# Kernel optimization log

Measured on AMD Instinct MI355X. Metric: run time of the kernel, lower is better.

Reference implementation:

```python
import jax, jax.numpy as jnp
import numpy as np


def _propagate(x, src, dst, norm, n):
    # PyG propagate with aggr='add': out[dst_e] += norm_e * x[src_e]
    return jax.ops.segment_sum(x[src] * norm[:, None], dst, num_segments=n)


def _dconv(x, w, b, row, col, norm_out, norm_in, n):
    # DConv with K=2: w has shape (2, 2, c_in, c_out)
    # k=0 term: identity for both diffusion directions
    h = x @ w[0, 0] + x @ w[1, 0]
    # k=1 term: 1-hop diffusion, forward edges and flipped edges
    tx_o = _propagate(x, row, col, norm_out, n)  # out-degree normalized walk
    tx_i = _propagate(x, col, row, norm_in, n)   # edge_index.flip([0]) walk
    h = h + tx_o @ w[0, 1] + tx_i @ w[1, 1]
    return h + b


def reference(x, edge_index, edge_weight, w_lin2, b_lin2, w_z, b_z, w_r, b_r, w_h, b_h, w_out, b_out):
    n = x.shape[0]
    row, col = edge_index[0], edge_index[1]
    # degrees from weighted adjacency (same as to_dense_adj row/col sums)
    deg_out = jax.ops.segment_sum(edge_weight, row, num_segments=n)
    deg_in = jax.ops.segment_sum(edge_weight, col, num_segments=n)
    norm_out = (1.0 / deg_out)[row]
    norm_in = (1.0 / deg_in)[row]

    h = x.reshape(n, -1)                      # Flatten: (n, 24)
    h = jax.nn.sigmoid(h @ w_lin2 + b_lin2)   # (n, hidden)

    # DCRNN GRU cell, hidden state initialized to zeros (single step)
    h0 = jnp.zeros_like(h)
    xh = jnp.concatenate([h, h0], axis=1)     # (n, 2*hidden)
    z = jax.nn.sigmoid(_dconv(xh, w_z, b_z, row, col, norm_out, norm_in, n))
    r = jax.nn.sigmoid(_dconv(xh, w_r, b_r, row, col, norm_out, norm_in, n))
    xhr = jnp.concatenate([h, h0 * r], axis=1)
    h_tilde = jnp.tanh(_dconv(xhr, w_h, b_h, row, col, norm_out, norm_in, n))
    h_new = z * h0 + (1.0 - z) * h_tilde

    return jax.nn.sigmoid(h_new) @ w_out + b_out  # (n, out_periods)


def setup_inputs() -> dict:
    key = jax.random.key(0)
    ks = jax.random.split(key, 12)
    N, DEG, HID, OUTP, WIN, HOR = 100000, 8, 64, 12, 2, 12
    E = N * DEG

    x = jax.random.normal(ks[0], (N, WIN, HOR), dtype=jnp.float32)

    # random edges + a ring so every node has out-degree>=1 and in-degree>=1
    e_rand = N * (DEG - 1)
    row_r = jax.random.randint(ks[1], (e_rand,), 0, N, dtype=jnp.int32)
    col_r = jax.random.randint(ks[2], (e_rand,), 0, N, dtype=jnp.int32)
    ring = jnp.arange(N, dtype=jnp.int32)
    row = jnp.concatenate([row_r, ring])
    col = jnp.concatenate([col_r, (ring + 1) % N])
    edge_index = jnp.stack([row, col])  # (2, E)
    edge_weight = jax.random.uniform(ks[3], (E,), minval=0.5, maxval=1.5, dtype=jnp.float32)

    def lin_w(k, fi, fo):
        return jax.random.normal(k, (fi, fo), jnp.float32) / np.float32(np.sqrt(fi))

    def dconv_w(k, cin, cout):
        return jax.random.normal(k, (2, 2, cin, cout), jnp.float32) / np.float32(np.sqrt(cin))

    cin = 2 * HID
    return {
        "x": x,
        "edge_index": edge_index,
        "edge_weight": edge_weight,
        "w_lin2": lin_w(ks[4], WIN * HOR, HID),
        "b_lin2": jnp.zeros((HID,), jnp.float32),
        "w_z": dconv_w(ks[5], cin, HID),
        "b_z": jnp.zeros((HID,), jnp.float32),
        "w_r": dconv_w(ks[6], cin, HID),
        "b_r": jnp.zeros((HID,), jnp.float32),
        "w_h": dconv_w(ks[7], cin, HID),
        "b_h": jnp.zeros((HID,), jnp.float32),
        "w_out": lin_w(ks[8], HID, OUTP),
        "b_out": jnp.zeros((OUTP,), jnp.float32),
    }
```

## Files before the change

kernel.cpp:

```cpp
#include <hip/hip_runtime.h>


typedef unsigned long long ull;
typedef unsigned short ushort;
typedef unsigned int uint;
typedef __attribute__((ext_vector_type(8))) short bf16x8;
typedef __attribute__((ext_vector_type(4))) float f32x4;

#define BSZ    64
#define CAP    768
#define CHUNK  4096
#define MAXBKT 2048

__device__ __forceinline__ float sigmoid_f(float x) {
    return 1.0f / (1.0f + __expf(-x));
}
__device__ __forceinline__ float tanh_f(float x) {
    float ax = fabsf(x);
    float e = __expf(-2.0f * ax);
    float t = (1.0f - e) / (1.0f + e);
    return copysignf(t, x);
}
__device__ __forceinline__ ushort f2bf(float f) {
    unsigned u = __float_as_uint(f);
    return (ushort)((u + 0x7FFF + ((u >> 16) & 1)) >> 16);
}
__device__ __forceinline__ float bf2f(ushort s) {
    return __uint_as_float(((unsigned)s) << 16);
}

__global__ void init_kernel(uint* __restrict__ gcur, int nbkt) {
    int t = blockIdx.x * 1024 + threadIdx.x;
    if (t < 2 * nbkt) gcur[t] = (uint)(t % nbkt) * CAP;
}

__global__ void __launch_bounds__(256) mega1_kernel(
        const int* __restrict__ row, const int* __restrict__ col,
        const float* __restrict__ ew, int E,
        uint* __restrict__ gcur, ull* __restrict__ pkbuf,
        int nbkt, int nslot,
        const float* __restrict__ x, const float* __restrict__ Wl,
        const float* __restrict__ bl, ushort* __restrict__ hb, int N,
        const float* __restrict__ wz, const float* __restrict__ bz,
        const float* __restrict__ wh, const float* __restrict__ bh,
        ushort* __restrict__ Wp, float* __restrict__ bc, int SB, int LB) {
    __shared__ float Ws[24 * 64];
    __shared__ float bs[64];
    __shared__ uint hist[MAXBKT];
    __shared__ uint base_s[MAXBKT];
    int bx = blockIdx.x;
    const int t = threadIdx.x;

    if (bx < SB) {
        const int d  = bx & 1;
        const int e0 = (bx >> 1) * CHUNK;
        const int* key = d ? row : col;
        const int* oth = d ? col : row;
        for (int i = t; i < nbkt; i += 256) hist[i] = 0;
        __syncthreads();
#pragma unroll
        for (int j = 0; j < CHUNK / 256; ++j) {
            int e = e0 + j * 256 + t;
            if (e < E) atomicAdd(&hist[key[e] >> 6], 1u);
        }
        __syncthreads();
        for (int i = t; i < nbkt; i += 256) {
            uint c = hist[i];
            base_s[i] = c ? atomicAdd(&gcur[d * nbkt + i], c) : 0u;
            hist[i] = 0;
        }
        __syncthreads();
#pragma unroll
        for (int j = 0; j < CHUNK / 256; ++j) {
            int e = e0 + j * 256 + t;
            if (e < E) {
                int k   = key[e];
                int bkt = k >> 6;
                uint w15 = (uint)(ew[e] * 16384.0f + 0.5f);
                uint s = base_s[bkt] + atomicAdd(&hist[bkt], 1u);
                if (s < ((uint)bkt + 1u) * CAP)
                    pkbuf[(size_t)d * nslot + s] =
                        ((ull)(uint)oth[e] << 32) |
                        ((uint)(k & (BSZ - 1)) << 15) | w15;
            }
        }
        return;
    }
    bx -= SB;
    if (bx < LB) {
        for (int i = t; i < 384; i += 256)
            ((float4*)Ws)[i] = ((const float4*)Wl)[i];
        if (t < 64) bs[t] = bl[t];
        __syncthreads();
        int gid = bx * 256 + t;
        int n = gid >> 6;
        int c = gid & 63;
        if (n >= N) return;
        const float* xr = x + (size_t)n * 24;
        float acc = bs[c];
#pragma unroll
        for (int k4 = 0; k4 < 6; ++k4) {
            float4 xv = *(const float4*)(xr + k4 * 4);
            acc = fmaf(xv.x, Ws[(k4 * 4 + 0) * 64 + c], acc);
            acc = fmaf(xv.y, Ws[(k4 * 4 + 1) * 64 + c], acc);
            acc = fmaf(xv.z, Ws[(k4 * 4 + 2) * 64 + c], acc);
            acc = fmaf(xv.w, Ws[(k4 * 4 + 3) * 64 + c], acc);
        }
        hb[(size_t)n * 64 + c] = f2bf(sigmoid_f(acc));
        return;
    }
    bx -= LB;
    int i = bx * 256 + t;
    if (bx == 0 && t < 128) bc[t] = (t < 64) ? bz[t] : bh[t - 64];
    if (i >= 6 * 8 * 64 * 8) return;
    int j    = i & 7;
    int lane = (i >> 3) & 63;
    int ct   = (i >> 9) & 7;
    int kt   = i >> 12;
    int k = kt * 32 + 8 * (lane >> 4) + j;
    int c = ct * 16 + (lane & 15);
    const float* w = (c < 64) ? wz : wh;
    int cc = c & 63;
    float v;
    if (k < 64)        v = w[(0 * 128 + k) * 64 + cc] + w[(2 * 128 + k) * 64 + cc];
    else if (k < 128)  v = w[(1 * 128 + (k - 64)) * 64 + cc];
    else               v = w[(3 * 128 + (k - 128)) * 64 + cc];
    Wp[i] = f2bf(v);
}

__global__ void __launch_bounds__(256) sort_kernel(
        const uint* __restrict__ gcur, const ull* __restrict__ pkbuf,
        uint* __restrict__ srt, int* __restrict__ beg, int* __restrict__ end,
        float* __restrict__ rdi, float* __restrict__ rdo,
        int nbkt, int nslot, int N) {
    __shared__ uint hist[BSZ];
    __shared__ uint cur[BSZ];
    __shared__ float sdeg[BSZ];
    const int b = blockIdx.x, d = blockIdx.y, t = threadIdx.x;
    if (t < BSZ) { hist[t] = 0; sdeg[t] = 0.0f; }
    __syncthreads();
    uint cnt = gcur[d * nbkt + b] - (uint)b * CAP;
    if (cnt > CAP) cnt = CAP;
    const ull* rec = pkbuf + (size_t)d * nslot + (size_t)b * CAP;
    for (uint i = t; i < cnt; i += 256) {
        ull r = rec[i];
        uint dl = (uint)(r >> 15) & (BSZ - 1);
        atomicAdd(&hist[dl], 1u);
        atomicAdd(&sdeg[dl], (float)(uint)(r & 0x7FFFu));
    }
    __syncthreads();
    if (t < BSZ) {
        int v = (int)hist[t];
        int x = v;
#pragma unroll
        for (int off = 1; off < BSZ; off <<= 1) {
            int y = __shfl_up(x, off, 64);
            if (t >= off) x += y;
        }
        uint p = (uint)(x - v);
        cur[t] = p;
        int n = b * BSZ + t;
        if (n < N) {
            beg[(size_t)d * N + n] = (int)((uint)b * CAP + p);
            end[(size_t)d * N + n] = (int)((uint)b * CAP + p + (uint)v);
            float s = sdeg[t];
            float rv = (s > 0.0f) ? (16384.0f / s) : 0.0f;
            if (d == 0) rdi[n] = rv;
            else        rdo[n] = rv;
        }
    }
    __syncthreads();
    uint* so = srt + (size_t)d * nslot + (size_t)b * CAP;
    for (uint i = t; i < cnt; i += 256) {
        ull r = rec[i];
        uint dl = (uint)(r >> 15) & (BSZ - 1);
        uint p = atomicAdd(&cur[dl], 1u);
        so[p] = (uint)(r >> 32);
    }
}

__global__ void __launch_bounds__(256) gather_kernel(
        const ushort* __restrict__ hb, const uint* __restrict__ srt,
        const int* __restrict__ beg, const int* __restrict__ end,
        const float* __restrict__ rdo, const float* __restrict__ rdi,
        ushort* __restrict__ pob, ushort* __restrict__ pib,
        int nslot, int N) {
    int n = blockIdx.x * 4 + (threadIdx.x >> 6);
    if (n >= N) return;
    const int lane = threadIdx.x & 63;
    const int g    = lane >> 4;
    const int cq   = (lane & 15) * 4;
    const int d    = blockIdx.y;
    const uint* s_ = srt + (size_t)d * nslot;
    int s0 = beg[(size_t)d * N + n];
    int s1 = end[(size_t)d * N + n];

    float a0 = 0.f, a1 = 0.f, a2 = 0.f, a3 = 0.f;
    for (int s = s0; s < s1; s += 8) {
        int sa = s + g, sb = s + 4 + g;
        int ia = (int)s_[(sa < s1) ? sa : s1 - 1];
        int ib = (int)s_[(sb < s1) ? sb : s1 - 1];
        float wa, wb;
        if (d == 0) {
            wa = (sa < s1) ? rdo[ia] : 0.0f;
            wb = (sb < s1) ? rdo[ib] : 0.0f;
        } else {
            wa = (sa < s1) ? 1.0f : 0.0f;
            wb = (sb < s1) ? 1.0f : 0.0f;
        }
        uint2 ha = *(const uint2*)(hb + (size_t)ia * 64 + cq);
        uint2 hc = *(const uint2*)(hb + (size_t)ib * 64 + cq);
        a0 = fmaf(__uint_as_float(ha.x << 16),         wa, a0);
        a1 = fmaf(__uint_as_float(ha.x & 0xFFFF0000u), wa, a1);
        a2 = fmaf(__uint_as_float(ha.y << 16),         wa, a2);
        a3 = fmaf(__uint_as_float(ha.y & 0xFFFF0000u), wa, a3);
        a0 = fmaf(__uint_as_float(hc.x << 16),         wb, a0);
        a1 = fmaf(__uint_as_float(hc.x & 0xFFFF0000u), wb, a1);
        a2 = fmaf(__uint_as_float(hc.y << 16),         wb, a2);
        a3 = fmaf(__uint_as_float(hc.y & 0xFFFF0000u), wb, a3);
    }
    a0 += __shfl_xor(a0, 16, 64); a0 += __shfl_xor(a0, 32, 64);
    a1 += __shfl_xor(a1, 16, 64); a1 += __shfl_xor(a1, 32, 64);
    a2 += __shfl_xor(a2, 16, 64); a2 += __shfl_xor(a2, 32, 64);
    a3 += __shfl_xor(a3, 16, 64); a3 += __shfl_xor(a3, 32, 64);

    if (lane < 16) {
        float m = (d == 0) ? 1.0f : rdi[n];
        uint lo = (uint)f2bf(a0 * m) | ((uint)f2bf(a1 * m) << 16);
        uint hi = (uint)f2bf(a2 * m) | ((uint)f2bf(a3 * m) << 16);
        ushort* dst = (d == 0 ? pob : pib) + (size_t)n * 64 + cq;
        *(uint2*)dst = make_uint2(lo, hi);
    }
}

__global__ void __launch_bounds__(256) gates_kernel(
        const ushort* __restrict__ hb, const ushort* __restrict__ pob,
        const ushort* __restrict__ pib, const ushort* __restrict__ Wp,
        const float* __restrict__ bc, const float* __restrict__ wout,
        const float* __restrict__ bout, float* __restrict__ out, int N) {
    __shared__ float sS[64 * 68];
    __shared__ float sWO[64 * 12];
    const int t    = threadIdx.x;
    const int w    = t >> 6;
    const int lane = t & 63;
    const int n0   = blockIdx.x * 64;

    for (int i = t; i < 64 * 12; i += 256) sWO[i] = wout[i];

    f32x4 acc[8];
#pragma unroll
    for (int ct = 0; ct < 8; ++ct) {
        float bcv = bc[ct * 16 + (lane & 15)];
        acc[ct] = (f32x4){bcv, bcv, bcv, bcv};
    }

    int arow = n0 + w * 16 + (lane & 15);
    if (arow >= N) arow = N - 1;
    const int g8 = (lane >> 4) * 8;
    const ushort* const srcs[3] = {hb, pob, pib};

#pragma unroll
    for (int kc = 0; kc < 6; ++kc) {
        const ushort* src = srcs[kc >> 1];
        bf16x8 a = *(const bf16x8*)(src + (size_t)arow * 64 + (kc & 1) * 32 + g8);
#pragma unroll
        for (int ct = 0; ct < 8; ++ct) {
            bf16x8 b = *(const bf16x8*)(Wp + (size_t)((kc * 8 + ct) * 64 + lane) * 8);
            acc[ct] = __builtin_amdgcn_mfma_f32_16x16x32_bf16(a, b, acc[ct], 0, 0, 0);
        }
    }

    const int rowbase = w * 16 + (lane >> 4) * 4;
    const int colbase = lane & 15;
#pragma unroll
    for (int ct = 0; ct < 4; ++ct) {
#pragma unroll
        for (int r = 0; r < 4; ++r) {
            float zv = sigmoid_f(acc[ct][r]);
            float ht = tanh_f(acc[ct + 4][r]);
            sS[(rowbase + r) * 68 + ct * 16 + colbase] =
                sigmoid_f((1.0f - zv) * ht);
        }
    }
    __syncthreads();

#pragma unroll
    for (int rr = 0; rr < 3; ++rr) {
        int o = rr * 256 + t;
        int node = o / 12;
        int j = o % 12;
        int n = n0 + node;
        if (n >= N) continue;
        float a = bout[j];
#pragma unroll 8
        for (int c2 = 0; c2 < 64; ++c2) a = fmaf(sS[node * 68 + c2], sWO[c2 * 12 + j], a);
        out[(size_t)n * 12 + j] = a;
    }
}

extern "C" void kernel_launch(void* const* d_in, const int* in_sizes, int n_in,
                              void* d_out, int out_size, void* d_ws, size_t ws_size,
                              hipStream_t stream) {
    const float* x      = (const float*)d_in[0];
    const int*   ei     = (const int*)  d_in[1];
    const float* ew     = (const float*)d_in[2];
    const float* w_lin2 = (const float*)d_in[3];
    const float* b_lin2 = (const float*)d_in[4];
    const float* w_z    = (const float*)d_in[5];
    const float* b_z    = (const float*)d_in[6];
    const float* w_h    = (const float*)d_in[9];
    const float* b_h    = (const float*)d_in[10];
    const float* w_out  = (const float*)d_in[11];
    const float* b_out  = (const float*)d_in[12];

    int N = in_sizes[0] / 24;
    int E = in_sizes[1] / 2;
    const int* row = ei;
    const int* col = ei + E;
    int nbkt  = (N + BSZ - 1) / BSZ;
    int nslot = nbkt * CAP;

    ull*    pkbuf = (ull*)d_ws;
    uint*   srt   = (uint*)(pkbuf + 2 * (size_t)nslot);
    ushort* hb    = (ushort*)(srt + 2 * (size_t)nslot);
    ushort* pob   = hb  + (size_t)N * 64;
    ushort* pib   = pob + (size_t)N * 64;
    ushort* Wp    = pib + (size_t)N * 64;
    float*  bc    = (float*)(Wp + 24576);
    float*  rdo   = bc + 128;
    float*  rdi   = rdo + N;
    int*    beg   = (int*)(rdi + N);
    int*    end   = beg + 2 * (size_t)N;
    uint*   gcur  = (uint*)(end + 2 * (size_t)N);

    int SB = 2 * ((E + CHUNK - 1) / CHUNK);
    int LB = (N * 64 + 255) / 256;
    int PB = (6 * 8 * 64 * 8 + 255) / 256;

    init_kernel<<<(2 * nbkt + 1023) / 1024, 1024, 0, stream>>>(gcur, nbkt);
    mega1_kernel<<<SB + LB + PB, 256, 0, stream>>>(
        row, col, ew, E, gcur, pkbuf, nbkt, nslot,
        x, w_lin2, b_lin2, hb, N,
        w_z, b_z, w_h, b_h, Wp, bc, SB, LB);
    sort_kernel<<<dim3(nbkt, 2), 256, 0, stream>>>(gcur, pkbuf, srt, beg, end,
                                                   rdi, rdo, nbkt, nslot, N);
    gather_kernel<<<dim3((N + 3) / 4, 2), 256, 0, stream>>>(hb, srt, beg, end,
                                                            rdo, rdi, pob, pib,
                                                            nslot, N);
    gates_kernel<<<(N + 63) / 64, 256, 0, stream>>>(hb, pob, pib, Wp, bc,
                                                    w_out, b_out, (float*)d_out, N);
}
```

Measured before the change: 164.8 us.

## Make gather kernel persistent with prefetched edge indices; pack beg/end; memset counters

The gather kernel becomes a grid-stride persistent kernel with a fixed 2048x2 grid. Each wave prefetches the next batch of source indices, including the first batch of the next node, while it processes the current batch, so the index load is no longer on the critical path of the feature gather. Begin and end offsets are packed into one int2 array, so each node needs a single load. The init kernel is replaced by hipMemsetAsync, with the bucket base now added when offsets are reserved. The partitioning CHUNK grows to 12288, which means fewer, larger histogram blocks. The cost is less wave-level parallelism in the gather and more register pressure.

```diff
diff --git a/kernel.cpp b/kernel.cpp
--- a/kernel.cpp
+++ b/kernel.cpp
@@ -9,7 +9,7 @@
 
 #define BSZ    64
 #define CAP    768
-#define CHUNK  4096
+#define CHUNK  12288
 #define MAXBKT 2048
 
 __device__ __forceinline__ float sigmoid_f(float x) {
@@ -24,14 +24,6 @@
 __device__ __forceinline__ ushort f2bf(float f) {
     unsigned u = __float_as_uint(f);
     return (ushort)((u + 0x7FFF + ((u >> 16) & 1)) >> 16);
-}
-__device__ __forceinline__ float bf2f(ushort s) {
-    return __uint_as_float(((unsigned)s) << 16);
-}
-
-__global__ void init_kernel(uint* __restrict__ gcur, int nbkt) {
-    int t = blockIdx.x * 1024 + threadIdx.x;
-    if (t < 2 * nbkt) gcur[t] = (uint)(t % nbkt) * CAP;
 }
 
 __global__ void __launch_bounds__(256) mega1_kernel(
@@ -66,7 +58,7 @@
         __syncthreads();
         for (int i = t; i < nbkt; i += 256) {
             uint c = hist[i];
-            base_s[i] = c ? atomicAdd(&gcur[d * nbkt + i], c) : 0u;
+            base_s[i] = c ? (uint)i * CAP + atomicAdd(&gcur[d * nbkt + i], c) : 0u;
             hist[i] = 0;
         }
         __syncthreads();
@@ -130,7 +122,7 @@
 
 __global__ void __launch_bounds__(256) sort_kernel(
         const uint* __restrict__ gcur, const ull* __restrict__ pkbuf,
-        uint* __restrict__ srt, int* __restrict__ beg, int* __restrict__ end,
+        uint* __restrict__ srt, int2* __restrict__ be,
         float* __restrict__ rdi, float* __restrict__ rdo,
         int nbkt, int nslot, int N) {
     __shared__ uint hist[BSZ];
@@ -139,7 +131,7 @@
     const int b = blockIdx.x, d = blockIdx.y, t = threadIdx.x;
     if (t < BSZ) { hist[t] = 0; sdeg[t] = 0.0f; }
     __syncthreads();
-    uint cnt = gcur[d * nbkt + b] - (uint)b * CAP;
+    uint cnt = gcur[d * nbkt + b];
     if (cnt > CAP) cnt = CAP;
     const ull* rec = pkbuf + (size_t)d * nslot + (size_t)b * CAP;
     for (uint i = t; i < cnt; i += 256) {
@@ -161,8 +153,9 @@
         cur[t] = p;
         int n = b * BSZ + t;
         if (n < N) {
-            beg[(size_t)d * N + n] = (int)((uint)b * CAP + p);
-            end[(size_t)d * N + n] = (int)((uint)b * CAP + p + (uint)v);
+            be[(size_t)d * N + n] =
+                make_int2((int)((uint)b * CAP + p),
+                          (int)((uint)b * CAP + p + (uint)v));
             float s = sdeg[t];
             float rv = (s > 0.0f) ? (16384.0f / s) : 0.0f;
             if (d == 0) rdi[n] = rv;
@@ -181,55 +174,77 @@
 
 __global__ void __launch_bounds__(256) gather_kernel(
         const ushort* __restrict__ hb, const uint* __restrict__ srt,
-        const int* __restrict__ beg, const int* __restrict__ end,
+        const int2* __restrict__ be,
         const float* __restrict__ rdo, const float* __restrict__ rdi,
         ushort* __restrict__ pob, ushort* __restrict__ pib,
         int nslot, int N) {
-    int n = blockIdx.x * 4 + (threadIdx.x >> 6);
-    if (n >= N) return;
     const int lane = threadIdx.x & 63;
     const int g    = lane >> 4;
     const int cq   = (lane & 15) * 4;
     const int d    = blockIdx.y;
-    const uint* s_ = srt + (size_t)d * nslot;
-    int s0 = beg[(size_t)d * N + n];
-    int s1 = end[(size_t)d * N + n];
-
-    float a0 = 0.f, a1 = 0.f, a2 = 0.f, a3 = 0.f;
-    for (int s = s0; s < s1; s += 8) {
-        int sa = s + g, sb = s + 4 + g;
-        int ia = (int)s_[(sa < s1) ? sa : s1 - 1];
-        int ib = (int)s_[(sb < s1) ? sb : s1 - 1];
-        float wa, wb;
-        if (d == 0) {
-            wa = (sa < s1) ? rdo[ia] : 0.0f;
-            wb = (sb < s1) ? rdo[ib] : 0.0f;
-        } else {
-            wa = (sa < s1) ? 1.0f : 0.0f;
-            wb = (sb < s1) ? 1.0f : 0.0f;
-        }
-        uint2 ha = *(const uint2*)(hb + (size_t)ia * 64 + cq);
-        uint2 hc = *(const uint2*)(hb + (size_t)ib * 64 + cq);
-        a0 = fmaf(__uint_as_float(ha.x << 16),         wa, a0);
-        a1 = fmaf(__uint_as_float(ha.x & 0xFFFF0000u), wa, a1);
-        a2 = fmaf(__uint_as_float(ha.y << 16),         wa, a2);
-        a3 = fmaf(__uint_as_float(ha.y & 0xFFFF0000u), wa, a3);
-        a0 = fmaf(__uint_as_float(hc.x << 16),         wb, a0);
-        a1 = fmaf(__uint_as_float(hc.x & 0xFFFF0000u), wb, a1);
-        a2 = fmaf(__uint_as_float(hc.y << 16),         wb, a2);
-        a3 = fmaf(__uint_as_float(hc.y & 0xFFFF0000u), wb, a3);
-    }
-    a0 += __shfl_xor(a0, 16, 64); a0 += __shfl_xor(a0, 32, 64);
-    a1 += __shfl_xor(a1, 16, 64); a1 += __shfl_xor(a1, 32, 64);
-    a2 += __shfl_xor(a2, 16, 64); a2 += __shfl_xor(a2, 32, 64);
-    a3 += __shfl_xor(a3, 16, 64); a3 += __shfl_xor(a3, 32, 64);
-
-    if (lane < 16) {
-        float m = (d == 0) ? 1.0f : rdi[n];
-        uint lo = (uint)f2bf(a0 * m) | ((uint)f2bf(a1 * m) << 16);
-        uint hi = (uint)f2bf(a2 * m) | ((uint)f2bf(a3 * m) << 16);
-        ushort* dst = (d == 0 ? pob : pib) + (size_t)n * 64 + cq;
-        *(uint2*)dst = make_uint2(lo, hi);
+    const uint* s_  = srt + (size_t)d * nslot;
+    const int2* be_ = be + (size_t)d * N;
+
+    int wid  = blockIdx.x * 4 + (threadIdx.x >> 6);
+    int step = gridDim.x * 4;
+    if (wid >= N) return;
+
+    int2 r0 = be_[wid];
+    uint ia = s_[min(r0.x + g,     r0.y - 1)];
+    uint ib = s_[min(r0.x + 4 + g, r0.y - 1)];
+
+    for (int n = wid; n < N; n += step) {
+        int nn = n + step;
+        bool has_next = (nn < N);
+        int2 r1 = r0;
+        if (has_next) r1 = be_[nn];
+
+        float a0 = 0.f, a1 = 0.f, a2 = 0.f, a3 = 0.f;
+        int s = r0.x, e = r0.y;
+        while (s < e) {
+            int sn = s + 8;
+            uint ia_n = ia, ib_n = ib;
+            if (sn < e) {
+                ia_n = s_[min(sn + g,     e - 1)];
+                ib_n = s_[min(sn + 4 + g, e - 1)];
+            } else if (has_next) {
+                ia_n = s_[min(r1.x + g,     r1.y - 1)];
+                ib_n = s_[min(r1.x + 4 + g, r1.y - 1)];
+            }
+            bool va = (s + g < e), vb = (s + 4 + g < e);
+            float wa, wb;
+            if (d == 0) {
+                wa = va ? rdo[ia] : 0.0f;
+                wb = vb ? rdo[ib] : 0.0f;
+            } else {
+                wa = va ? 1.0f : 0.0f;
+                wb = vb ? 1.0f : 0.0f;
+            }
+            uint2 ha = *(const uint2*)(hb + (size_t)ia * 64 + cq);
+            uint2 hc = *(const uint2*)(hb + (size_t)ib * 64 + cq);
+            a0 = fmaf(__uint_as_float(ha.x << 16),         wa, a0);
+            a1 = fmaf(__uint_as_float(ha.x & 0xFFFF0000u), wa, a1);
+            a2 = fmaf(__uint_as_float(ha.y << 16),         wa, a2);
+            a3 = fmaf(__uint_as_float(ha.y & 0xFFFF0000u), wa, a3);
+            a0 = fmaf(__uint_as_float(hc.x << 16),         wb, a0);
+            a1 = fmaf(__uint_as_float(hc.x & 0xFFFF0000u), wb, a1);
+            a2 = fmaf(__uint_as_float(hc.y << 16),         wb, a2);
+            a3 = fmaf(__uint_as_float(hc.y & 0xFFFF0000u), wb, a3);
+            s = sn; ia = ia_n; ib = ib_n;
+        }
+        a0 += __shfl_xor(a0, 16, 64); a0 += __shfl_xor(a0, 32, 64);
+        a1 += __shfl_xor(a1, 16, 64); a1 += __shfl_xor(a1, 32, 64);
+        a2 += __shfl_xor(a2, 16, 64); a2 += __shfl_xor(a2, 32, 64);
+        a3 += __shfl_xor(a3, 16, 64); a3 += __shfl_xor(a3, 32, 64);
+
+        if (lane < 16) {
+            float m = (d == 0) ? 1.0f : rdi[n];
+            uint lo = (uint)f2bf(a0 * m) | ((uint)f2bf(a1 * m) << 16);
+            uint hi = (uint)f2bf(a2 * m) | ((uint)f2bf(a3 * m) << 16);
+            ushort* dst = (d == 0 ? pob : pib) + (size_t)n * 64 + cq;
+            *(uint2*)dst = make_uint2(lo, hi);
+        }
+        r0 = r1;
     }
 }
 
@@ -329,24 +344,22 @@
     float*  bc    = (float*)(Wp + 24576);
     float*  rdo   = bc + 128;
     float*  rdi   = rdo + N;
-    int*    beg   = (int*)(rdi + N);
-    int*    end   = beg + 2 * (size_t)N;
-    uint*   gcur  = (uint*)(end + 2 * (size_t)N);
+    int2*   be    = (int2*)(rdi + N);
+    uint*   gcur  = (uint*)(be + 2 * (size_t)N);
 
     int SB = 2 * ((E + CHUNK - 1) / CHUNK);
     int LB = (N * 64 + 255) / 256;
     int PB = (6 * 8 * 64 * 8 + 255) / 256;
 
-    init_kernel<<<(2 * nbkt + 1023) / 1024, 1024, 0, stream>>>(gcur, nbkt);
+    hipMemsetAsync(gcur, 0, 2 * (size_t)nbkt * sizeof(uint), stream);
     mega1_kernel<<<SB + LB + PB, 256, 0, stream>>>(
         row, col, ew, E, gcur, pkbuf, nbkt, nslot,
         x, w_lin2, b_lin2, hb, N,
         w_z, b_z, w_h, b_h, Wp, bc, SB, LB);
-    sort_kernel<<<dim3(nbkt, 2), 256, 0, stream>>>(gcur, pkbuf, srt, beg, end,
+    sort_kernel<<<dim3(nbkt, 2), 256, 0, stream>>>(gcur, pkbuf, srt, be,
                                                    rdi, rdo, nbkt, nslot, N);
-    gather_kernel<<<dim3((N + 3) / 4, 2), 256, 0, stream>>>(hb, srt, beg, end,
-                                                            rdo, rdi, pob, pib,
-                                                            nslot, N);
+    gather_kernel<<<dim3(2048, 2), 256, 0, stream>>>(hb, srt, be, rdo, rdi,
+                                                     pob, pib, nslot, N);
     gates_kernel<<<(N + 63) / 64, 256, 0, stream>>>(hb, pob, pib, Wp, bc,
                                                     w_out, b_out, (float*)d_out, N);
 }
```

After: 160.3 us. 1.03x faster.
